# Performance work log

Measured on AMD Instinct MI355X. Metric: run time of the kernel, lower is better.

Reference implementation:

```python
import jax, jax.numpy as jnp
import numpy as np

EPS = 1e-5
NUM_HEADS = 16
NUM_KV_HEADS = 4
HEAD_DIM = 64
TOP_K = 2


def _layer_norm(x, w, b):
    m = jnp.mean(x, axis=-1, keepdims=True)
    v = jnp.mean((x - m) ** 2, axis=-1, keepdims=True)
    return (x - m) * jax.lax.rsqrt(v + EPS) * w + b


def setup_inputs() -> dict:
    key = jax.random.key(0)
    ks = jax.random.split(key, 8)
    S, B, H = 2048, 1, 1024
    E, F = 8, 4096
    q_per_kv = NUM_HEADS // NUM_KV_HEADS
    qkv_out = NUM_KV_HEADS * (q_per_kv + 2) * HEAD_DIM  # 1536

    def w(k, shape, scale=0.02):
        return jax.random.normal(k, shape, dtype=jnp.float32) * scale

    return {
        "hidden_states": jax.random.normal(ks[0], (S, B, H), dtype=jnp.float32),
        "ln1_weight": jnp.ones((H,), jnp.float32),
        "ln1_bias": jnp.zeros((H,), jnp.float32),
        "ln2_weight": jnp.ones((H,), jnp.float32),
        "ln2_bias": jnp.zeros((H,), jnp.float32),
        "qkv_weight": w(ks[1], (qkv_out, H)),
        "proj_weight": w(ks[2], (H, H)),
        "router_weight": w(ks[3], (H, E)),
        "moe_w1": w(ks[4], (E, H, F)),
        "moe_w2": w(ks[5], (E, F, H)),
    }


def reference(hidden_states, ln1_weight, ln1_bias, ln2_weight, ln2_bias,
              qkv_weight, proj_weight, router_weight, moe_w1, moe_w2):
    S, B, H = hidden_states.shape
    D = HEAD_DIM
    Hq, Hkv = NUM_HEADS, NUM_KV_HEADS
    g = Hq // Hkv                      # queries per kv head (GQA group)
    scale = 1.0 / np.sqrt(D)

    # ---- attention block ----
    ln1_out = _layer_norm(hidden_states, ln1_weight, ln1_bias)
    qkv = ln1_out @ qkv_weight.T                      # [S,B,Hkv*(g+2)*D]
    qkv = qkv.reshape(S, B, Hkv, (g + 2) * D)
    q = qkv[..., : g * D].reshape(S, B, Hq, D)        # [S,B,Hq,D]
    k = qkv[..., g * D : (g + 1) * D]                 # [S,B,Hkv,D]
    v = qkv[..., (g + 1) * D :]                       # [S,B,Hkv,D]

    # cp_size == 1 -> Ulysses all-to-alls are identity
    q_bf = q.transpose(1, 2, 0, 3).reshape(B, Hkv, g, S, D)  # [B,Hkv,g,S,D]
    k_bf = k.transpose(1, 2, 0, 3)                           # [B,Hkv,S,D]
    v_bf = v.transpose(1, 2, 0, 3)

    scores = jnp.einsum("bkgsd,bktd->bkgst", q_bf, k_bf) * scale
    causal = jnp.tril(jnp.ones((S, S), dtype=bool))
    scores = jnp.where(causal, scores, jnp.float32(-1e30))
    probs = jax.nn.softmax(scores, axis=-1)
    attn = jnp.einsum("bkgst,bktd->bkgsd", probs, v_bf)      # [B,Hkv,g,S,D]
    attn = attn.reshape(B, Hq, S, D).transpose(2, 0, 1, 3).reshape(S, B, Hq * D)

    proj_out = attn @ proj_weight.T
    hidden_after_attn = hidden_states + proj_out

    # ---- MoE block ----
    ln2_out = _layer_norm(hidden_after_attn, ln2_weight, ln2_bias)
    x = ln2_out.reshape(-1, H)                        # [T,H]
    T = x.shape[0]

    logits = x @ router_weight                        # [T,E] (fp32)
    rprobs = jax.nn.softmax(logits, axis=-1)
    top_p, top_i = jax.lax.top_k(rprobs, TOP_K)       # [T,k]
    top_p = top_p / jnp.sum(top_p, axis=-1, keepdims=True)

    # ep_size == 1: dispatch/sort/all-to-all are a pure permutation; compute
    # each expert densely over all tokens, then gather the routed outputs
    # (identical math to sort+grouped-GEMM+unsort).
    fc1 = jnp.einsum("th,ehf->etf", x, moe_w1)        # [E,T,F]
    act = jax.nn.gelu(fc1, approximate=False)
    y = jnp.einsum("etf,efh->eth", act, moe_w2)       # [E,T,H]

    tok = jnp.arange(T)[:, None]                      # [T,1]
    gathered = y[top_i, tok, :]                       # [T,k,H]
    moe_out = jnp.sum(gathered * top_p[..., None], axis=1)  # [T,H]

    return hidden_after_attn + moe_out.reshape(S, B, H)
```

## Files before the change

kernel.cpp:

```cpp
#include <hip/hip_runtime.h>
#include <cstdint>
#include <cstddef>

typedef unsigned short u16;
typedef __attribute__((ext_vector_type(8))) short bf16x8;
typedef __attribute__((ext_vector_type(4))) float f32x4;

#define MFMA16(a, b, c) __builtin_amdgcn_mfma_f32_16x16x32_bf16((a), (b), (c), 0, 0, 0)

__device__ __forceinline__ u16 f2bf(float f) {
  uint32_t u = __builtin_bit_cast(uint32_t, f);
  u += 0x7fffu + ((u >> 16) & 1u);
  return (u16)(u >> 16);
}
__device__ __forceinline__ float bf2f(u16 h) {
  uint32_t u = ((uint32_t)h) << 16;
  return __builtin_bit_cast(float, u);
}

__device__ __forceinline__ void gload_lds16(const void* g, void* l) {
  __builtin_amdgcn_global_load_lds(
      (const __attribute__((address_space(1))) uint32_t*)g,
      (__attribute__((address_space(3))) uint32_t*)l, 16, 0, 0);
}

template<bool WRITE_LO, bool WRITE_F32>
__launch_bounds__(256)
__global__ void ln_kernel(const float* __restrict__ in,
                          const float* __restrict__ w, const float* __restrict__ b,
                          u16* __restrict__ out_hi, u16* __restrict__ out_lo,
                          float* __restrict__ out_f32)
{
  int row = blockIdx.x;
  int tid = threadIdx.x;
  const float* x = in + (size_t)row * 1024;
  float4 v = *(const float4*)(x + tid * 4);
  float s  = v.x + v.y + v.z + v.w;
  float s2 = v.x*v.x + v.y*v.y + v.z*v.z + v.w*v.w;
  #pragma unroll
  for (int d = 1; d < 64; d <<= 1) { s += __shfl_xor(s, d); s2 += __shfl_xor(s2, d); }
  __shared__ float red[2][4];
  int wid = tid >> 6;
  if ((tid & 63) == 0) { red[0][wid] = s; red[1][wid] = s2; }
  __syncthreads();
  s  = red[0][0] + red[0][1] + red[0][2] + red[0][3];
  s2 = red[1][0] + red[1][1] + red[1][2] + red[1][3];
  float mean = s * (1.0f / 1024.0f);
  float var  = s2 * (1.0f / 1024.0f) - mean * mean;
  float rstd = rsqrtf(var + 1e-5f);
  float vv[4] = {v.x, v.y, v.z, v.w};
  #pragma unroll
  for (int j = 0; j < 4; ++j) {
    int c = tid * 4 + j;
    float y = (vv[j] - mean) * rstd * w[c] + b[c];
    size_t idx = (size_t)row * 1024 + c;
    u16 hb = f2bf(y);
    out_hi[idx] = hb;
    if (WRITE_LO)  out_lo[idx] = f2bf(y - bf2f(hb));
    if (WRITE_F32) out_f32[idx] = y;
  }
}

__global__ void convert_split_kernel(const float* __restrict__ in,
                                     u16* __restrict__ hi, u16* __restrict__ lo, int n4)
{
  int i = blockIdx.x * blockDim.x + threadIdx.x;
  if (i >= n4) return;
  float4 v = *(const float4*)(in + (size_t)i * 4);
  float a[4] = {v.x, v.y, v.z, v.w};
  u16 hh[4], ll[4];
  #pragma unroll
  for (int j = 0; j < 4; ++j) {
    hh[j] = f2bf(a[j]);
    ll[j] = f2bf(a[j] - bf2f(hh[j]));
  }
  uint2 hp, lp;
  hp.x = (uint32_t)hh[0] | ((uint32_t)hh[1] << 16);
  hp.y = (uint32_t)hh[2] | ((uint32_t)hh[3] << 16);
  lp.x = (uint32_t)ll[0] | ((uint32_t)ll[1] << 16);
  lp.y = (uint32_t)ll[2] | ((uint32_t)ll[3] << 16);
  *(uint2*)(hi + (size_t)i * 4) = hp;
  *(uint2*)(lo + (size_t)i * 4) = lp;
}

__global__ void transpose_convert_kernel(const float* __restrict__ in, u16* __restrict__ out,
                                         int R, int C)
{
  __shared__ float t[32][33];
  size_t ebase = (size_t)blockIdx.z * R * C;
  int c0 = blockIdx.x * 32, r0 = blockIdx.y * 32;
  int tx = threadIdx.x, ty = threadIdx.y;
  #pragma unroll
  for (int i = 0; i < 4; ++i)
    t[ty + 8*i][tx] = in[ebase + (size_t)(r0 + ty + 8*i) * C + (c0 + tx)];
  __syncthreads();
  #pragma unroll
  for (int i = 0; i < 4; ++i)
    out[ebase + (size_t)(c0 + ty + 8*i) * R + (r0 + tx)] = f2bf(t[tx][ty + 8*i]);
}

__global__ void vtrans_kernel(const u16* __restrict__ qkv, u16* __restrict__ vT)
{
  __shared__ u16 t[32][34];
  int kvh = blockIdx.z;
  int s0 = blockIdx.x * 32, d0 = blockIdx.y * 32;
  int tx = threadIdx.x, ty = threadIdx.y;
  #pragma unroll
  for (int i = 0; i < 4; ++i)
    t[ty + 8*i][tx] = qkv[(size_t)(s0 + ty + 8*i) * 1536 + kvh * 384 + 320 + d0 + tx];
  __syncthreads();
  #pragma unroll
  for (int i = 0; i < 4; ++i)
    vT[((size_t)kvh * 64 + d0 + ty + 8*i) * 2048 + (s0 + tx)] = t[tx][ty + 8*i];
}

template<int MODE, bool SPLIT>
__launch_bounds__(256, SPLIT ? 2 : 4)
__global__ void gemm_kernel(const u16* __restrict__ Ahi, const u16* __restrict__ Alo,
                            const u16* __restrict__ Bhi, const u16* __restrict__ Blo,
                            int N, int K,
                            u16* __restrict__ Cb_hi, u16* __restrict__ Cb_lo,
                            float* __restrict__ Cf, const float* __restrict__ resid,
                            const int* __restrict__ tok_of_pair,
                            const int* __restrict__ counts, const int* __restrict__ prefix)
{
  int bn = blockIdx.x, bm = blockIdx.y;
  int row_base = 0;
  int count = 1 << 30;
  int kbeg = 0, kend = K;
  if constexpr (MODE >= 2) {
    int L = blockIdx.x + 32 * (blockIdx.y + 16 * blockIdx.z);
    int xcd = L & 7, idx = L >> 3;
    int e;
    if constexpr (MODE == 2) {
      bn = idx & 31;
      e  = xcd;
      bm = (idx >> 5) & 15;
    } else {
      bn = idx & 7;
      int G = xcd * 64 + (idx >> 3);
      int s = G >> 7;
      int rem = G & 127;
      e  = rem >> 4;
      bm = rem & 15;
      int kc = K >> 2;
      kbeg = s * kc; kend = kbeg + kc;
      Cf += (size_t)s * 4096 * 1024;
    }
    count = counts[e];
    if (bm * 128 >= count) return;
    row_base = prefix[e];
    Bhi += (size_t)e * N * K;
  }
  __shared__ u16 As[2][SPLIT ? 2 : 1][128 * 32];
  __shared__ u16 Bs[2][SPLIT ? 2 : 1][128 * 32];

  int tid = threadIdx.x;
  int lane = tid & 63;
  int lo16 = lane & 15, hi4 = lane >> 4;
  int wid = tid >> 6, wr = wid >> 1, wc = wid & 1;

  const u16* gA[2][2];
  const u16* gB[2][2];
  int eidx[2];
  #pragma unroll
  for (int q = 0; q < 2; ++q) {
    int el = (q * 256 + tid) * 8;
    int r = el >> 5, c = el & 31;
    eidx[q] = el;
    if constexpr (MODE == 2) {
      int lim = count - bm * 128 - 1;
      int lr = r < lim ? r : lim;
      int token = tok_of_pair[row_base + bm * 128 + lr];
      gA[q][0] = Ahi + (size_t)token * K + c;
    } else if constexpr (MODE == 3) {
      int lim = count - bm * 128 - 1;
      int lr = r < lim ? r : lim;
      gA[q][0] = Ahi + (size_t)(row_base + bm * 128 + lr) * K + c;
    } else {
      gA[q][0] = Ahi + (size_t)(bm * 128 + r) * K + c;
      if constexpr (SPLIT) gA[q][1] = Alo + (size_t)(bm * 128 + r) * K + c;
    }
    gB[q][0] = Bhi + (size_t)(bn * 128 + r) * K + c;
    if constexpr (SPLIT) gB[q][1] = Blo + (size_t)(bn * 128 + r) * K + c;
  }

  auto stage = [&](int buf, int k0) {
    #pragma unroll
    for (int q = 0; q < 2; ++q) {
      gload_lds16(gA[q][0] + k0, &As[buf][0][eidx[q]]);
      gload_lds16(gB[q][0] + k0, &Bs[buf][0][eidx[q]]);
      if constexpr (SPLIT) {
        gload_lds16(gA[q][1] + k0, &As[buf][1][eidx[q]]);
        gload_lds16(gB[q][1] + k0, &Bs[buf][1][eidx[q]]);
      }
    }
  };

  const f32x4 zf = {0.f, 0.f, 0.f, 0.f};
  f32x4 acc[4][4];
  #pragma unroll
  for (int m = 0; m < 4; ++m)
    #pragma unroll
    for (int n = 0; n < 4; ++n) acc[m][n] = zf;

  stage(0, kbeg);
  __syncthreads();

  int cur = 0;
  for (int k0 = kbeg; k0 < kend; k0 += 32, cur ^= 1) {
    if (k0 + 32 < kend) stage(cur ^ 1, k0 + 32);

    bf16x8 a0[4], b0[4], a1[4], b1[4];
    #pragma unroll
    for (int m = 0; m < 4; ++m)
      a0[m] = *(const bf16x8*)&As[cur][0][(wr * 64 + m * 16 + lo16) * 32 + hi4 * 8];
    #pragma unroll
    for (int n = 0; n < 4; ++n)
      b0[n] = *(const bf16x8*)&Bs[cur][0][(wc * 64 + n * 16 + lo16) * 32 + hi4 * 8];
    if constexpr (SPLIT) {
      #pragma unroll
      for (int m = 0; m < 4; ++m)
        a1[m] = *(const bf16x8*)&As[cur][1][(wr * 64 + m * 16 + lo16) * 32 + hi4 * 8];
      #pragma unroll
      for (int n = 0; n < 4; ++n)
        b1[n] = *(const bf16x8*)&Bs[cur][1][(wc * 64 + n * 16 + lo16) * 32 + hi4 * 8];
    }
    #pragma unroll
    for (int m = 0; m < 4; ++m)
      #pragma unroll
      for (int n = 0; n < 4; ++n) {
        acc[m][n] = MFMA16(a0[m], b0[n], acc[m][n]);
        if constexpr (SPLIT) {
          acc[m][n] = MFMA16(a0[m], b1[n], acc[m][n]);
          acc[m][n] = MFMA16(a1[m], b0[n], acc[m][n]);
        }
      }
    __syncthreads();
  }

  #pragma unroll
  for (int m = 0; m < 4; ++m)
    #pragma unroll
    for (int n = 0; n < 4; ++n)
      #pragma unroll
      for (int r = 0; r < 4; ++r) {
        int lr = wr * 64 + m * 16 + hi4 * 4 + r;
        int col = bn * 128 + wc * 64 + n * 16 + lo16;
        float v = acc[m][n][r];
        if constexpr (MODE == 0) {
          size_t idx = (size_t)(bm * 128 + lr) * N + col;
          u16 hb = f2bf(v);
          Cb_hi[idx] = hb;
          Cb_lo[idx] = f2bf(v - bf2f(hb));
        } else if constexpr (MODE == 1) {
          size_t idx = (size_t)(bm * 128 + lr) * N + col;
          Cf[idx] = v + resid[idx];
        } else if constexpr (MODE == 2) {
          if (bm * 128 + lr < count) {
            size_t idx = (size_t)(row_base + bm * 128 + lr) * N + col;
            float g = 0.5f * v * (1.0f + erff(v * 0.70710678118654752f));
            Cb_hi[idx] = f2bf(g);
          }
        } else {
          if (bm * 128 + lr < count) {
            size_t idx = (size_t)(row_base + bm * 128 + lr) * N + col;
            Cf[idx] = v;
          }
        }
      }
}

struct QState {
  bf16x8 qf[2][2];
  f32x4 o[4];
  float m_r[4], l_r[4];
  int qrow[4];
};

__device__ __forceinline__ void qstate_init(QState& S,
    const u16* qkv_hi, const u16* qkv_lo, int q0w, int qoff, int lo16, int hi4)
{
  const u16* ph = qkv_hi + (size_t)(q0w + lo16) * 1536 + qoff + hi4 * 8;
  const u16* pl = qkv_lo + (size_t)(q0w + lo16) * 1536 + qoff + hi4 * 8;
  S.qf[0][0] = *(const bf16x8*)ph;  S.qf[0][1] = *(const bf16x8*)(ph + 32);
  S.qf[1][0] = *(const bf16x8*)pl;  S.qf[1][1] = *(const bf16x8*)(pl + 32);
  const f32x4 zf = {0.f, 0.f, 0.f, 0.f};
  #pragma unroll
  for (int r = 0; r < 4; ++r) { S.m_r[r] = -INFINITY; S.l_r[r] = 0.f; S.qrow[r] = q0w + hi4 * 4 + r; }
  #pragma unroll
  for (int n = 0; n < 4; ++n) S.o[n] = zf;
}

__device__ __forceinline__ void attn_tile(QState& S, int kv0,
    const u16* Ks0, const u16* Ks1, const u16* Vs0, const u16* Vs1,
    u16* Ps0, u16* Ps1, int lo16, int hi4)
{
  const f32x4 zf = {0.f, 0.f, 0.f, 0.f};
  f32x4 sc[4];
  __builtin_amdgcn_s_setprio(1);
  #pragma unroll
  for (int c2 = 0; c2 < 4; ++c2) {
    sc[c2] = zf;
    int krow = c2 * 16 + lo16;
    const u16* kb  = &Ks0[krow * 64];
    const u16* kbl = &Ks1[krow * 64];
    bf16x8 kh0 = *(const bf16x8*)&kb [((hi4    ) ^ (krow & 7)) * 8];
    bf16x8 kh1 = *(const bf16x8*)&kb [((hi4 + 4) ^ (krow & 7)) * 8];
    bf16x8 kl0 = *(const bf16x8*)&kbl[((hi4    ) ^ (krow & 7)) * 8];
    bf16x8 kl1 = *(const bf16x8*)&kbl[((hi4 + 4) ^ (krow & 7)) * 8];
    sc[c2] = MFMA16(S.qf[0][0], kh0, sc[c2]);
    sc[c2] = MFMA16(S.qf[0][1], kh1, sc[c2]);
    sc[c2] = MFMA16(S.qf[0][0], kl0, sc[c2]);
    sc[c2] = MFMA16(S.qf[0][1], kl1, sc[c2]);
    sc[c2] = MFMA16(S.qf[1][0], kh0, sc[c2]);
    sc[c2] = MFMA16(S.qf[1][1], kh1, sc[c2]);
  }
  __builtin_amdgcn_s_setprio(0);

  float tmax[4] = {-INFINITY, -INFINITY, -INFINITY, -INFINITY};
  #pragma unroll
  for (int c2 = 0; c2 < 4; ++c2) {
    int kv = kv0 + c2 * 16 + lo16;
    #pragma unroll
    for (int r = 0; r < 4; ++r) {
      float sv = sc[c2][r] * 0.125f;
      if (kv > S.qrow[r]) sv = -1e30f;
      sc[c2][r] = sv;
      tmax[r] = fmaxf(tmax[r], sv);
    }
  }
  #pragma unroll
  for (int d = 1; d < 16; d <<= 1)
    #pragma unroll
    for (int r = 0; r < 4; ++r)
      tmax[r] = fmaxf(tmax[r], __shfl_xor(tmax[r], d));
  float rs[4], rowsum[4];
  #pragma unroll
  for (int r = 0; r < 4; ++r) {
    float mn = fmaxf(S.m_r[r], tmax[r]);
    rs[r] = __expf(S.m_r[r] - mn);
    S.m_r[r] = mn;
    rowsum[r] = 0.f;
  }
  #pragma unroll
  for (int c2 = 0; c2 < 4; ++c2)
    #pragma unroll
    for (int r = 0; r < 4; ++r) {
      float pv = __expf(sc[c2][r] - S.m_r[r]);
      sc[c2][r] = pv;
      rowsum[r] += pv;
    }
  #pragma unroll
  for (int d = 1; d < 16; d <<= 1)
    #pragma unroll
    for (int r = 0; r < 4; ++r)
      rowsum[r] += __shfl_xor(rowsum[r], d);
  #pragma unroll
  for (int r = 0; r < 4; ++r) S.l_r[r] = S.l_r[r] * rs[r] + rowsum[r];
  #pragma unroll
  for (int n = 0; n < 4; ++n)
    #pragma unroll
    for (int r = 0; r < 4; ++r) S.o[n][r] *= rs[r];

  #pragma unroll
  for (int c2 = 0; c2 < 4; ++c2)
    #pragma unroll
    for (int r = 0; r < 4; ++r) {
      float pv = sc[c2][r];
      u16 ph = f2bf(pv);
      int pidx = (hi4 * 4 + r) * 72 + c2 * 16 + lo16;
      Ps0[pidx] = ph;
      Ps1[pidx] = f2bf(pv - bf2f(ph));
    }

  __builtin_amdgcn_s_setprio(1);
  #pragma unroll
  for (int k2 = 0; k2 < 2; ++k2) {
    bf16x8 pah = *(const bf16x8*)&Ps0[lo16 * 72 + k2 * 32 + hi4 * 8];
    bf16x8 pal = *(const bf16x8*)&Ps1[lo16 * 72 + k2 * 32 + hi4 * 8];
    #pragma unroll
    for (int n = 0; n < 4; ++n) {
      int vrow = n * 16 + lo16;
      bf16x8 vh = *(const bf16x8*)&Vs0[vrow * 64 + (((k2 * 4 + hi4) ^ (vrow & 7))) * 8];
      bf16x8 vl = *(const bf16x8*)&Vs1[vrow * 64 + (((k2 * 4 + hi4) ^ (vrow & 7))) * 8];
      S.o[n] = MFMA16(pah, vh, S.o[n]);
      S.o[n] = MFMA16(pah, vl, S.o[n]);
      S.o[n] = MFMA16(pal, vh, S.o[n]);
    }
  }
  __builtin_amdgcn_s_setprio(0);
}

__device__ __forceinline__ void qstate_out(QState& S, int q0w, int h,
    u16* out_hi, u16* out_lo, int lo16, int hi4)
{
  #pragma unroll
  for (int n = 0; n < 4; ++n)
    #pragma unroll
    for (int r = 0; r < 4; ++r) {
      float v = S.o[n][r] / S.l_r[r];
      size_t idx = (size_t)(q0w + hi4 * 4 + r) * 1024 + h * 64 + n * 16 + lo16;
      u16 hb = f2bf(v);
      out_hi[idx] = hb;
      out_lo[idx] = f2bf(v - bf2f(hb));
    }
}

__launch_bounds__(256)
__global__ void attn_kernel(const u16* __restrict__ qkv_hi, const u16* __restrict__ qkv_lo,
                            const u16* __restrict__ vT_hi, const u16* __restrict__ vT_lo,
                            u16* __restrict__ out_hi, u16* __restrict__ out_lo)
{
  int id = blockIdx.y * 32 + blockIdx.x;
  int h = id & 15;
  int j = (id >> 4) & 15;
  int qb = (id < 256) ? (31 - j) : j;
  int kvh = h >> 2, gi = h & 3;
  int tid = threadIdx.x;
  int lane = tid & 63;
  int w = tid >> 6;
  int lo16 = lane & 15, hi4 = lane >> 4;
  int q0w = qb * 64 + w * 16;
  int qoff = kvh * 384 + gi * 64;
  int koff = kvh * 384 + 256;

  __shared__ u16 Ks[2][64 * 64];
  __shared__ u16 Vs[2][64 * 64];
  __shared__ u16 Ps[2][4][16 * 72];
  u16* Ps0 = &Ps[0][w][0];
  u16* Ps1 = &Ps[1][w][0];

  QState S;
  qstate_init(S, qkv_hi, qkv_lo, q0w, qoff, lo16, hi4);

  for (int t = 0; t <= qb; ++t) {
    int kv0 = t * 64;
    __syncthreads();
    #pragma unroll
    for (int it = 0; it < 2; ++it) {
      int u = it * 256 + tid;
      int row = u >> 3, ch = u & 7;
      int d = (ch ^ (row & 7)) * 8;
      *(uint4*)&Ks[0][row * 64 + d] = *(const uint4*)(qkv_hi + (size_t)(kv0 + row) * 1536 + koff + ch * 8);
      *(uint4*)&Ks[1][row * 64 + d] = *(const uint4*)(qkv_lo + (size_t)(kv0 + row) * 1536 + koff + ch * 8);
      *(uint4*)&Vs[0][row * 64 + d] = *(const uint4*)(vT_hi + ((size_t)kvh * 64 + row) * 2048 + kv0 + ch * 8);
      *(uint4*)&Vs[1][row * 64 + d] = *(const uint4*)(vT_lo + ((size_t)kvh * 64 + row) * 2048 + kv0 + ch * 8);
    }
    __syncthreads();

    attn_tile(S, kv0, Ks[0], Ks[1], Vs[0], Vs[1], Ps0, Ps1, lo16, hi4);
  }

  qstate_out(S, q0w, h, out_hi, out_lo, lo16, hi4);
}

__launch_bounds__(64)
__global__ void router_kernel(const float* __restrict__ x, const float* __restrict__ rw,
                              int* __restrict__ counts, int* __restrict__ esel,
                              int* __restrict__ slotsel, float* __restrict__ wsel)
{
  int t = blockIdx.x;
  int l = threadIdx.x;
  float acc[8] = {0.f, 0.f, 0.f, 0.f, 0.f, 0.f, 0.f, 0.f};
  const float* xr = x + (size_t)t * 1024;
  for (int hh = l; hh < 1024; hh += 64) {
    float xv = xr[hh];
    const float* wp = rw + hh * 8;
    #pragma unroll
    for (int e = 0; e < 8; ++e) acc[e] = fmaf(xv, wp[e], acc[e]);
  }
  #pragma unroll
  for (int e = 0; e < 8; ++e)
    #pragma unroll
    for (int d = 1; d < 64; d <<= 1) acc[e] += __shfl_xor(acc[e], d);
  if (l == 0) {
    int e1 = 0;
    #pragma unroll
    for (int e = 1; e < 8; ++e) if (acc[e] > acc[e1]) e1 = e;
    int e2 = -1;
    #pragma unroll
    for (int e = 0; e < 8; ++e) {
      if (e == e1) continue;
      if (e2 < 0 || acc[e] > acc[e2]) e2 = e;
    }
    float p1 = 1.0f / (1.0f + expf(acc[e2] - acc[e1]));
    float p2 = 1.0f - p1;
    int s1 = atomicAdd(&counts[e1], 1);
    int s2 = atomicAdd(&counts[e2], 1);
    esel[t * 2] = e1; esel[t * 2 + 1] = e2;
    slotsel[t * 2] = s1; slotsel[t * 2 + 1] = s2;
    wsel[t * 2] = p1; wsel[t * 2 + 1] = p2;
  }
}

__global__ void build_lists_kernel(const int* __restrict__ counts, int* __restrict__ prefix,
                                   const int* __restrict__ esel, const int* __restrict__ slotsel,
                                   int* __restrict__ tok_of_pair, int* __restrict__ pair_idx)
{
  __shared__ int pfx[8];
  if (threadIdx.x == 0) {
    int a = 0;
    for (int e = 0; e < 8; ++e) { pfx[e] = a; prefix[e] = a; a += counts[e]; }
  }
  __syncthreads();
  for (int t = threadIdx.x; t < 2048; t += 256) {
    #pragma unroll
    for (int k = 0; k < 2; ++k) {
      int e = esel[t * 2 + k];
      int row = pfx[e] + slotsel[t * 2 + k];
      tok_of_pair[row] = t;
      pair_idx[t * 2 + k] = row;
    }
  }
}

__launch_bounds__(256)
__global__ void final_kernel(const float* __restrict__ hattn, const float* __restrict__ y,
                             const int* __restrict__ pair_idx, const float* __restrict__ wsel,
                             float* __restrict__ out)
{
  int t = blockIdx.x;
  int c = threadIdx.x * 4;
  int p0 = pair_idx[t * 2], p1 = pair_idx[t * 2 + 1];
  float w0 = wsel[t * 2], w1 = wsel[t * 2 + 1];
  float4 a = *(const float4*)(hattn + (size_t)t * 1024 + c);
  float y0x = 0.f, y0y = 0.f, y0z = 0.f, y0w = 0.f;
  float y1x = 0.f, y1y = 0.f, y1z = 0.f, y1w = 0.f;
  #pragma unroll
  for (int s = 0; s < 4; ++s) {
    const float* base = y + (size_t)s * 4096 * 1024;
    float4 v0 = *(const float4*)(base + (size_t)p0 * 1024 + c);
    float4 v1 = *(const float4*)(base + (size_t)p1 * 1024 + c);
    y0x += v0.x; y0y += v0.y; y0z += v0.z; y0w += v0.w;
    y1x += v1.x; y1y += v1.y; y1z += v1.z; y1w += v1.w;
  }
  float4 r;
  r.x = a.x + w0 * y0x + w1 * y1x;
  r.y = a.y + w0 * y0y + w1 * y1y;
  r.z = a.z + w0 * y0z + w1 * y1z;
  r.w = a.w + w0 * y0w + w1 * y1w;
  *(float4*)(out + (size_t)t * 1024 + c) = r;
}

extern "C" void kernel_launch(void* const* d_in, const int* in_sizes, int n_in,
                              void* d_out, int out_size, void* d_ws, size_t ws_size,
                              hipStream_t stream)
{
  const float* hidden   = (const float*)d_in[0];
  const float* ln1_w    = (const float*)d_in[1];
  const float* ln1_b    = (const float*)d_in[2];
  const float* ln2_w    = (const float*)d_in[3];
  const float* ln2_b    = (const float*)d_in[4];
  const float* qkv_w    = (const float*)d_in[5];
  const float* proj_w   = (const float*)d_in[6];
  const float* router_w = (const float*)d_in[7];
  const float* moe_w1   = (const float*)d_in[8];
  const float* moe_w2   = (const float*)d_in[9];
  float* out = (float*)d_out;

  char* ws = (char*)d_ws;
  size_t off = 0;
  auto alloc = [&](size_t bytes) -> void* {
    void* p = (void*)(ws + off);
    off += (bytes + 255) & ~(size_t)255;
    return p;
  };

  u16* wT      = (u16*)alloc(8ull * 4096 * 1024 * 2);
  float* hattn = (float*)alloc(2048ull * 1024 * 4);
  u16* x_hi    = (u16*)alloc(2048ull * 1024 * 2);
  u16* act     = (u16*)alloc(4096ull * 4096 * 2);
  float* ybuf  = (float*)alloc(4ull * 4096 * 1024 * 4);

  char* ov = (char*)ybuf;
  size_t oo = 0;
  auto oalloc = [&](size_t bytes) -> void* {
    void* p = (void*)(ov + oo);
    oo += (bytes + 255) & ~(size_t)255;
    return p;
  };
  u16* ln1_hi  = (u16*)oalloc(2048ull * 1024 * 2);
  u16* ln1_lo  = (u16*)oalloc(2048ull * 1024 * 2);
  u16* qw_hi   = (u16*)oalloc(1536ull * 1024 * 2);
  u16* qw_lo   = (u16*)oalloc(1536ull * 1024 * 2);
  u16* pw_hi   = (u16*)oalloc(1024ull * 1024 * 2);
  u16* pw_lo   = (u16*)oalloc(1024ull * 1024 * 2);
  u16* qkv_hi  = (u16*)oalloc(2048ull * 1536 * 2);
  u16* qkv_lo  = (u16*)oalloc(2048ull * 1536 * 2);
  u16* vt_hi   = (u16*)oalloc(4ull * 64 * 2048 * 2);
  u16* vt_lo   = (u16*)oalloc(4ull * 64 * 2048 * 2);
  u16* at_hi   = (u16*)oalloc(2048ull * 1024 * 2);
  u16* at_lo   = (u16*)oalloc(2048ull * 1024 * 2);
  float* x_f32 = (float*)oalloc(2048ull * 1024 * 4);

  int* counts  = (int*)alloc(8 * 4);
  int* prefix  = (int*)alloc(8 * 4);
  int* esel    = (int*)alloc(2048ull * 2 * 4);
  int* slotsel = (int*)alloc(2048ull * 2 * 4);
  int* topair  = (int*)alloc(4096ull * 4);
  int* pairidx = (int*)alloc(2048ull * 2 * 4);
  float* wsel  = (float*)alloc(2048ull * 2 * 4);

  hipMemsetAsync(counts, 0, 8 * 4, stream);

  ln_kernel<true, false><<<2048, 256, 0, stream>>>(hidden, ln1_w, ln1_b, ln1_hi, ln1_lo, nullptr);

  convert_split_kernel<<<1536, 256, 0, stream>>>(qkv_w, qw_hi, qw_lo, 1536 * 1024 / 4);
  convert_split_kernel<<<1024, 256, 0, stream>>>(proj_w, pw_hi, pw_lo, 1024 * 1024 / 4);

  gemm_kernel<0, true><<<dim3(12, 16, 1), 256, 0, stream>>>(
      ln1_hi, ln1_lo, qw_hi, qw_lo, 1536, 1024,
      qkv_hi, qkv_lo, nullptr, nullptr, nullptr, nullptr, nullptr);

  vtrans_kernel<<<dim3(64, 2, 4), dim3(32, 8), 0, stream>>>(qkv_hi, vt_hi);
  vtrans_kernel<<<dim3(64, 2, 4), dim3(32, 8), 0, stream>>>(qkv_lo, vt_lo);

  attn_kernel<<<dim3(32, 16), 256, 0, stream>>>(qkv_hi, qkv_lo, vt_hi, vt_lo, at_hi, at_lo);

  gemm_kernel<1, true><<<dim3(8, 16, 1), 256, 0, stream>>>(
      at_hi, at_lo, pw_hi, pw_lo, 1024, 1024,
      nullptr, nullptr, hattn, hidden, nullptr, nullptr, nullptr);

  ln_kernel<false, true><<<2048, 256, 0, stream>>>(hattn, ln2_w, ln2_b, x_hi, nullptr, x_f32);

  router_kernel<<<2048, 64, 0, stream>>>(x_f32, router_w, counts, esel, slotsel, wsel);
  build_lists_kernel<<<1, 256, 0, stream>>>(counts, prefix, esel, slotsel, topair, pairidx);

  transpose_convert_kernel<<<dim3(128, 32, 8), dim3(32, 8), 0, stream>>>(moe_w1, wT, 1024, 4096);

  gemm_kernel<2, false><<<dim3(32, 16, 8), 256, 0, stream>>>(
      x_hi, nullptr, wT, nullptr, 4096, 1024,
      act, nullptr, nullptr, nullptr, topair, counts, prefix);

  transpose_convert_kernel<<<dim3(32, 128, 8), dim3(32, 8), 0, stream>>>(moe_w2, wT, 4096, 1024);

  gemm_kernel<3, false><<<dim3(32, 16, 8), 256, 0, stream>>>(
      act, nullptr, wT, nullptr, 1024, 4096,
      nullptr, nullptr, ybuf, nullptr, topair, counts, prefix);

  final_kernel<<<2048, 256, 0, stream>>>(hattn, ybuf, pairidx, wsel, out);
}
```

Baseline: 490.9 us.

## Triple-buffer LDS staging in non-split GEMM with explicit vmcnt waits

For the non-split GEMM path, LDS staging moves from two buffers to three, so global-to-LDS loads run two K-tiles ahead. Each iteration uses explicit s_waitcnt vmcnt plus a bare s_barrier instead of __syncthreads, waiting only for the tile about to be read. The goal is more load latency hidden behind MFMA work and cheaper synchronisation. The larger LDS footprint forces the launch-bounds occupancy hint down from 4 to 3 blocks per CU, which may reduce latency hiding across blocks.

```diff
diff --git a/kernel.cpp b/kernel.cpp
--- a/kernel.cpp
+++ b/kernel.cpp
@@ -115,7 +115,7 @@
 }
 
 template<int MODE, bool SPLIT>
-__launch_bounds__(256, SPLIT ? 2 : 4)
+__launch_bounds__(256, SPLIT ? 2 : 3)
 __global__ void gemm_kernel(const u16* __restrict__ Ahi, const u16* __restrict__ Alo,
                             const u16* __restrict__ Bhi, const u16* __restrict__ Blo,
                             int N, int K,
@@ -152,8 +152,8 @@
     row_base = prefix[e];
     Bhi += (size_t)e * N * K;
   }
-  __shared__ u16 As[2][SPLIT ? 2 : 1][128 * 32];
-  __shared__ u16 Bs[2][SPLIT ? 2 : 1][128 * 32];
+  __shared__ u16 As[SPLIT ? 2 : 3][SPLIT ? 2 : 1][128 * 32];
+  __shared__ u16 Bs[SPLIT ? 2 : 3][SPLIT ? 2 : 1][128 * 32];
 
   int tid = threadIdx.x;
   int lane = tid & 63;
@@ -204,39 +204,72 @@
     #pragma unroll
     for (int n = 0; n < 4; ++n) acc[m][n] = zf;
 
-  stage(0, kbeg);
-  __syncthreads();
-
-  int cur = 0;
-  for (int k0 = kbeg; k0 < kend; k0 += 32, cur ^= 1) {
-    if (k0 + 32 < kend) stage(cur ^ 1, k0 + 32);
-
-    bf16x8 a0[4], b0[4], a1[4], b1[4];
-    #pragma unroll
-    for (int m = 0; m < 4; ++m)
-      a0[m] = *(const bf16x8*)&As[cur][0][(wr * 64 + m * 16 + lo16) * 32 + hi4 * 8];
-    #pragma unroll
-    for (int n = 0; n < 4; ++n)
-      b0[n] = *(const bf16x8*)&Bs[cur][0][(wc * 64 + n * 16 + lo16) * 32 + hi4 * 8];
-    if constexpr (SPLIT) {
+  if constexpr (!SPLIT) {
+    const int nt = (kend - kbeg) >> 5;
+    stage(0, kbeg);
+    if (nt > 1) {
+      stage(1, kbeg + 32);
+      asm volatile("s_waitcnt vmcnt(4)" ::: "memory");
+    } else {
+      asm volatile("s_waitcnt vmcnt(0)" ::: "memory");
+    }
+    __builtin_amdgcn_s_barrier();
+
+    int rb = 0, sb = 2;
+    for (int t = 0; t < nt; ++t) {
+      if (t + 2 < nt) stage(sb, kbeg + (t + 2) * 32);
+
+      bf16x8 a0[4], b0[4];
+      #pragma unroll
+      for (int m = 0; m < 4; ++m)
+        a0[m] = *(const bf16x8*)&As[rb][0][(wr * 64 + m * 16 + lo16) * 32 + hi4 * 8];
+      #pragma unroll
+      for (int n = 0; n < 4; ++n)
+        b0[n] = *(const bf16x8*)&Bs[rb][0][(wc * 64 + n * 16 + lo16) * 32 + hi4 * 8];
+      #pragma unroll
+      for (int m = 0; m < 4; ++m)
+        #pragma unroll
+        for (int n = 0; n < 4; ++n)
+          acc[m][n] = MFMA16(a0[m], b0[n], acc[m][n]);
+
+      if (t + 1 < nt) {
+        if (t + 2 < nt) asm volatile("s_waitcnt vmcnt(4)" ::: "memory");
+        else            asm volatile("s_waitcnt vmcnt(0)" ::: "memory");
+        __builtin_amdgcn_s_barrier();
+      }
+      rb = (rb == 2) ? 0 : rb + 1;
+      sb = (sb == 2) ? 0 : sb + 1;
+    }
+  } else {
+    stage(0, kbeg);
+    __syncthreads();
+    int cur = 0;
+    for (int k0 = kbeg; k0 < kend; k0 += 32, cur ^= 1) {
+      if (k0 + 32 < kend) stage(cur ^ 1, k0 + 32);
+
+      bf16x8 a0[4], b0[4], a1[4], b1[4];
+      #pragma unroll
+      for (int m = 0; m < 4; ++m)
+        a0[m] = *(const bf16x8*)&As[cur][0][(wr * 64 + m * 16 + lo16) * 32 + hi4 * 8];
+      #pragma unroll
+      for (int n = 0; n < 4; ++n)
+        b0[n] = *(const bf16x8*)&Bs[cur][0][(wc * 64 + n * 16 + lo16) * 32 + hi4 * 8];
       #pragma unroll
       for (int m = 0; m < 4; ++m)
         a1[m] = *(const bf16x8*)&As[cur][1][(wr * 64 + m * 16 + lo16) * 32 + hi4 * 8];
       #pragma unroll
       for (int n = 0; n < 4; ++n)
         b1[n] = *(const bf16x8*)&Bs[cur][1][(wc * 64 + n * 16 + lo16) * 32 + hi4 * 8];
-    }
-    #pragma unroll
-    for (int m = 0; m < 4; ++m)
-      #pragma unroll
-      for (int n = 0; n < 4; ++n) {
-        acc[m][n] = MFMA16(a0[m], b0[n], acc[m][n]);
-        if constexpr (SPLIT) {
+      #pragma unroll
+      for (int m = 0; m < 4; ++m)
+        #pragma unroll
+        for (int n = 0; n < 4; ++n) {
+          acc[m][n] = MFMA16(a0[m], b0[n], acc[m][n]);
           acc[m][n] = MFMA16(a0[m], b1[n], acc[m][n]);
           acc[m][n] = MFMA16(a1[m], b0[n], acc[m][n]);
         }
-      }
-    __syncthreads();
+      __syncthreads();
+    }
   }
 
   #pragma unroll
```

After: 486.8 us. No clear change (-0.8%).
